# Kernel optimization log

Hardware: AMD Instinct MI355X
Metric: run time of the kernel (lower is better)

Reference implementation:

```python
import jax, jax.numpy as jnp
import numpy as np

NEG_SLOPE = 0.2

def setup_inputs() -> dict:
    key = jax.random.key(0)
    k1, k2, k3 = jax.random.split(key, 3)
    N, d, attn = 1024, 256, 256
    H = jax.random.normal(k1, (N, d), dtype=jnp.float32)
    # nn.Linear(2*d, attn, bias=False).weight has shape [attn, 2*d]
    W = jax.random.normal(k2, (attn, 2 * d), dtype=jnp.float32) * 0.05
    a = jax.random.normal(k3, (attn, 1), dtype=jnp.float32) * 0.05
    return {"H": H, "W": W, "a": a}

def reference(H, W, a):
    # Faithful to: E = leakyrelu(Linear(cat[H_i, H_j])); scores = E @ a; alpha = softmax(scores, dim=1); out = alpha @ H
    # Decompose W into halves acting on H_i and H_j to avoid the N x N x 2d concat:
    d = H.shape[1]
    W1, W2 = W[:, :d], W[:, d:]          # each [attn, d]
    Wh1 = H @ W1.T                        # [N, attn] (contribution of H_i)
    Wh2 = H @ W2.T                        # [N, attn] (contribution of H_j)
    E = jax.nn.leaky_relu(Wh1[:, None, :] + Wh2[None, :, :], NEG_SLOPE)  # [N, N, attn]
    scores = jnp.einsum('ijk,ko->ij', E, a)   # [N, N]
    alpha = jax.nn.softmax(scores, axis=1)    # softmax over j (dim=1)
    return alpha @ H                          # [N, d] weighted sum of H_j
```

## Files before the change

kernel.cpp:

```cpp
#include <hip/hip_runtime.h>


#define HALF 524288

__global__ __launch_bounds__(256) void k1_gemm_wh(const float* __restrict__ H,
                                                  const float* __restrict__ W,
                                                  float* __restrict__ Whp) {
    __shared__ float As[64][36];
    __shared__ float Bs[32][36];
    const int bi = blockIdx.x, bm = blockIdx.y, bz = blockIdx.z;
    const int t = threadIdx.x;
    const int ti = t >> 4, tj = t & 15;
    const int i0 = ti * 4;
    const int half = bm >> 3;
    const int kbase = bz * 128;
    float acc[4][2] = {};
    for (int kc = 0; kc < 128; kc += 32) {
        const int kg = kbase + kc;
        {
            const int r = t >> 2, c = (t & 3) * 8;
            *(float4*)&As[r][c] = *(const float4*)&H[(bi * 64 + r) * 256 + kg + c];
            *(float4*)&As[r][c + 4] =
                *(const float4*)&H[(bi * 64 + r) * 256 + kg + c + 4];
        }
        {
            const int r = t >> 3, c = (t & 7) * 4;
            const int wrow = (bm * 32 + r) & 255;
            *(float4*)&Bs[r][c] =
                *(const float4*)&W[wrow * 512 + half * 256 + kg + c];
        }
        __syncthreads();
#pragma unroll
        for (int k = 0; k < 32; k += 4) {
            float4 a[4], b[2];
#pragma unroll
            for (int r = 0; r < 4; ++r) a[r] = *(const float4*)&As[i0 + r][k];
#pragma unroll
            for (int c = 0; c < 2; ++c) b[c] = *(const float4*)&Bs[tj + 16 * c][k];
#pragma unroll
            for (int r = 0; r < 4; ++r)
#pragma unroll
                for (int c = 0; c < 2; ++c) {
                    acc[r][c] = fmaf(a[r].x, b[c].x, acc[r][c]);
                    acc[r][c] = fmaf(a[r].y, b[c].y, acc[r][c]);
                    acc[r][c] = fmaf(a[r].z, b[c].z, acc[r][c]);
                    acc[r][c] = fmaf(a[r].w, b[c].w, acc[r][c]);
                }
        }
        __syncthreads();
    }
    float* dst = Whp + (size_t)bz * HALF;
#pragma unroll
    for (int r = 0; r < 4; ++r)
#pragma unroll
        for (int c = 0; c < 2; ++c)
            dst[(size_t)(bi * 64 + i0 + r) * 512 + bm * 32 + tj + 16 * c] = acc[r][c];
}

__global__ __launch_bounds__(256) void k1b_s2(const float* __restrict__ Whp,
                                              const float* __restrict__ a,
                                              float* __restrict__ s2) {
    const int t = threadIdx.x;
    const int lane = t & 63, w = t >> 6;
    const int row = blockIdx.x * 4 + w;
    const size_t off = (size_t)row * 512 + 256 + lane * 4;
    float4 x0 = *(const float4*)&Whp[off];
    float4 x1 = *(const float4*)&Whp[HALF + off];
    float4 av = *(const float4*)&a[lane * 4];
    float d = (x0.x + x1.x) * av.x + (x0.y + x1.y) * av.y +
              (x0.z + x1.z) * av.z + (x0.w + x1.w) * av.w;
#pragma unroll
    for (int o = 32; o > 0; o >>= 1) d += __shfl_xor(d, o);
    if (lane == 0) s2[row] = 0.6f * d;
}

__global__ __launch_bounds__(256) void kF_flash(const float* __restrict__ Whp,
                                                const float* __restrict__ a,
                                                const float* __restrict__ s2,
                                                const float* __restrict__ H,
                                                float* __restrict__ avp,
                                                float* __restrict__ mbuf,
                                                float* __restrict__ lbuf) {
    __shared__ float X1[32][68];
    __shared__ float X2[64][68];
    __shared__ float P[32][68];
    __shared__ float bsh[256];
    const int bi = blockIdx.x, bj = blockIdx.y;
    const int t = threadIdx.x;
    const int ti = t >> 4, tj = t & 15;
    const int i0 = ti * 2;
    if (t < 64) {
        float4 av = *(const float4*)&a[t * 4];
        *(float4*)&bsh[t * 4] =
            make_float4(0.4f * av.x, 0.4f * av.y, 0.4f * av.z, 0.4f * av.w);
    }
    float acc[2][4] = {};
    for (int mc = 0; mc < 256; mc += 64) {
        {
            const int r = t >> 3, c = (t & 7) * 8;
            const size_t g = (size_t)(bi * 32 + r) * 512 + mc + c;
            float4 p0 = *(const float4*)&Whp[g];
            float4 p1 = *(const float4*)&Whp[HALF + g];
            *(float4*)&X1[r][c] =
                make_float4(p0.x + p1.x, p0.y + p1.y, p0.z + p1.z, p0.w + p1.w);
            float4 q0 = *(const float4*)&Whp[g + 4];
            float4 q1 = *(const float4*)&Whp[HALF + g + 4];
            *(float4*)&X1[r][c + 4] =
                make_float4(q0.x + q1.x, q0.y + q1.y, q0.z + q1.z, q0.w + q1.w);
        }
        {
            const int r = t >> 2, c = (t & 3) * 16;
            const size_t g = (size_t)(bj * 64 + r) * 512 + 256 + mc + c;
#pragma unroll
            for (int q = 0; q < 4; ++q) {
                float4 p0 = *(const float4*)&Whp[g + q * 4];
                float4 p1 = *(const float4*)&Whp[HALF + g + q * 4];
                *(float4*)&X2[r][c + q * 4] = make_float4(
                    p0.x + p1.x, p0.y + p1.y, p0.z + p1.z, p0.w + p1.w);
            }
        }
        __syncthreads();
#pragma unroll
        for (int k = 0; k < 64; k += 4) {
            float4 x1[2], x2[4];
#pragma unroll
            for (int r = 0; r < 2; ++r) x1[r] = *(const float4*)&X1[i0 + r][k];
#pragma unroll
            for (int c = 0; c < 4; ++c) x2[c] = *(const float4*)&X2[tj + 16 * c][k];
            const float4 bv = *(const float4*)&bsh[mc + k];
#pragma unroll
            for (int r = 0; r < 2; ++r)
#pragma unroll
                for (int c = 0; c < 4; ++c) {
                    acc[r][c] = fmaf(fabsf(x1[r].x + x2[c].x), bv.x, acc[r][c]);
                    acc[r][c] = fmaf(fabsf(x1[r].y + x2[c].y), bv.y, acc[r][c]);
                    acc[r][c] = fmaf(fabsf(x1[r].z + x2[c].z), bv.z, acc[r][c]);
                    acc[r][c] = fmaf(fabsf(x1[r].w + x2[c].w), bv.w, acc[r][c]);
                }
        }
        __syncthreads();
    }
#pragma unroll
    for (int c = 0; c < 4; ++c) {
        const float sv = s2[bj * 64 + tj + 16 * c];
        acc[0][c] += sv;
        acc[1][c] += sv;
    }
#pragma unroll
    for (int r = 0; r < 2; ++r) {
        float mm = fmaxf(fmaxf(acc[r][0], acc[r][1]), fmaxf(acc[r][2], acc[r][3]));
        mm = fmaxf(mm, __shfl_xor(mm, 1));
        mm = fmaxf(mm, __shfl_xor(mm, 2));
        mm = fmaxf(mm, __shfl_xor(mm, 4));
        mm = fmaxf(mm, __shfl_xor(mm, 8));
        float l0 = 0.f;
#pragma unroll
        for (int c = 0; c < 4; ++c) {
            acc[r][c] = __expf(acc[r][c] - mm);
            l0 += acc[r][c];
        }
        l0 += __shfl_xor(l0, 1);
        l0 += __shfl_xor(l0, 2);
        l0 += __shfl_xor(l0, 4);
        l0 += __shfl_xor(l0, 8);
#pragma unroll
        for (int c = 0; c < 4; ++c) P[i0 + r][tj + 16 * c] = acc[r][c];
        if (tj == 0) {
            const int gi = bi * 32 + i0 + r;
            mbuf[bj * 1024 + gi] = mm;
            lbuf[bj * 1024 + gi] = l0;
        }
    }
    __syncthreads();
    for (int cc = 0; cc < 256; cc += 64) {
        {
            const int r = t >> 2, c = (t & 3) * 16;
            const size_t g = (size_t)(bj * 64 + r) * 256 + cc + c;
#pragma unroll
            for (int q = 0; q < 4; ++q)
                *(float4*)&X2[r][c + q * 4] = *(const float4*)&H[g + q * 4];
        }
        __syncthreads();
        float acc2[2][4] = {};
#pragma unroll
        for (int jj = 0; jj < 64; jj += 4) {
            float4 pv[2], h[4];
#pragma unroll
            for (int r = 0; r < 2; ++r) pv[r] = *(const float4*)&P[i0 + r][jj];
#pragma unroll
            for (int q = 0; q < 4; ++q) h[q] = *(const float4*)&X2[jj + q][tj * 4];
#pragma unroll
            for (int r = 0; r < 2; ++r) {
                acc2[r][0] = fmaf(pv[r].x, h[0].x, acc2[r][0]);
                acc2[r][1] = fmaf(pv[r].x, h[0].y, acc2[r][1]);
                acc2[r][2] = fmaf(pv[r].x, h[0].z, acc2[r][2]);
                acc2[r][3] = fmaf(pv[r].x, h[0].w, acc2[r][3]);
                acc2[r][0] = fmaf(pv[r].y, h[1].x, acc2[r][0]);
                acc2[r][1] = fmaf(pv[r].y, h[1].y, acc2[r][1]);
                acc2[r][2] = fmaf(pv[r].y, h[1].z, acc2[r][2]);
                acc2[r][3] = fmaf(pv[r].y, h[1].w, acc2[r][3]);
                acc2[r][0] = fmaf(pv[r].z, h[2].x, acc2[r][0]);
                acc2[r][1] = fmaf(pv[r].z, h[2].y, acc2[r][1]);
                acc2[r][2] = fmaf(pv[r].z, h[2].z, acc2[r][2]);
                acc2[r][3] = fmaf(pv[r].z, h[2].w, acc2[r][3]);
                acc2[r][0] = fmaf(pv[r].w, h[3].x, acc2[r][0]);
                acc2[r][1] = fmaf(pv[r].w, h[3].y, acc2[r][1]);
                acc2[r][2] = fmaf(pv[r].w, h[3].z, acc2[r][2]);
                acc2[r][3] = fmaf(pv[r].w, h[3].w, acc2[r][3]);
            }
        }
#pragma unroll
        for (int r = 0; r < 2; ++r) {
            *(float4*)&avp[(size_t)bj * 262144 + (size_t)(bi * 32 + i0 + r) * 256 +
                           cc + tj * 4] =
                make_float4(acc2[r][0], acc2[r][1], acc2[r][2], acc2[r][3]);
        }
        __syncthreads();
    }
}

__global__ __launch_bounds__(256) void kM_merge(const float* __restrict__ avp,
                                                const float* __restrict__ mbuf,
                                                const float* __restrict__ lbuf,
                                                float* __restrict__ out) {
    const int t = threadIdx.x;
    const int i = blockIdx.x * 4 + (t >> 6);
    const int c0 = (t & 63) * 4;
    float ms[16], es[16];
    float M = -1e30f;
#pragma unroll
    for (int s = 0; s < 16; ++s) {
        ms[s] = mbuf[s * 1024 + i];
        M = fmaxf(M, ms[s]);
    }
    float L = 0.f;
#pragma unroll
    for (int s = 0; s < 16; ++s) {
        es[s] = __expf(ms[s] - M);
        L = fmaf(es[s], lbuf[s * 1024 + i], L);
    }
    const float inv = 1.0f / L;
    float4 o = make_float4(0.f, 0.f, 0.f, 0.f);
#pragma unroll
    for (int s = 0; s < 16; ++s) {
        float4 p = *(const float4*)&avp[(size_t)s * 262144 + (size_t)i * 256 + c0];
        o.x = fmaf(es[s], p.x, o.x);
        o.y = fmaf(es[s], p.y, o.y);
        o.z = fmaf(es[s], p.z, o.z);
        o.w = fmaf(es[s], p.w, o.w);
    }
    o.x *= inv; o.y *= inv; o.z *= inv; o.w *= inv;
    *(float4*)&out[(size_t)i * 256 + c0] = o;
}

extern "C" void kernel_launch(void* const* d_in, const int* in_sizes, int n_in,
                              void* d_out, int out_size, void* d_ws, size_t ws_size,
                              hipStream_t stream) {
    const float* H = (const float*)d_in[0];
    const float* W = (const float*)d_in[1];
    const float* a = (const float*)d_in[2];
    float* out = (float*)d_out;
    float* ws = (float*)d_ws;

    float* avp = ws;
    float* mbuf = ws + (4u << 20);
    float* lbuf = mbuf + 16384;
    float* Whp = lbuf + 16384;
    float* s2 = Whp + 2 * HALF;

    hipLaunchKernelGGL(k1_gemm_wh, dim3(16, 16, 2), dim3(256), 0, stream, H, W, Whp);
    hipLaunchKernelGGL(k1b_s2, dim3(256), dim3(256), 0, stream, Whp, a, s2);
    hipLaunchKernelGGL(kF_flash, dim3(32, 16), dim3(256), 0, stream, Whp, a, s2, H,
                       avp, mbuf, lbuf);
    hipLaunchKernelGGL(kM_merge, dim3(256), dim3(256), 0, stream, avp, mbuf, lbuf, out);
}
```

Before: 58.86 us.

## Pre-merge split-K partials and double-buffer flash kernel LDS tiles with register prefetch

The split-K partial sums of Wh are now added once in a dedicated merge kernel, which also computes s2, so the flash kernel reads a single Wh buffer instead of two partials per tile. The flash kernel double-buffers its X1/X2 and H tiles in shared memory and prefetches the next chunk into registers while computing the current one. Explicit waitcnt/barrier macros replace __syncthreads, and the s2 loads are hoisted. Whp now aliases the avp workspace, which is safe only because Whp is consumed before avp is written. The costs are more LDS per block, which may lower occupancy, and higher register pressure.

```diff
diff --git a/kernel.cpp b/kernel.cpp
--- a/kernel.cpp
+++ b/kernel.cpp
@@ -2,6 +2,21 @@
 
 
 #define HALF 524288
+#define LDW 68
+
+#define FENCE_BAR() do {                                   \
+    __builtin_amdgcn_sched_barrier(0);                     \
+    asm volatile("s_waitcnt lgkmcnt(0)" ::: "memory");     \
+    __builtin_amdgcn_s_barrier();                          \
+    __builtin_amdgcn_sched_barrier(0);                     \
+} while (0)
+
+#define BAR_ONLY() do {                                    \
+    __builtin_amdgcn_sched_barrier(0);                     \
+    asm volatile("s_waitcnt lgkmcnt(0)" ::: "memory");     \
+    __builtin_amdgcn_s_barrier();                          \
+    __builtin_amdgcn_sched_barrier(0);                     \
+} while (0)
 
 __global__ __launch_bounds__(256) void k1_gemm_wh(const float* __restrict__ H,
                                                   const float* __restrict__ W,
@@ -57,77 +72,104 @@
             dst[(size_t)(bi * 64 + i0 + r) * 512 + bm * 32 + tj + 16 * c] = acc[r][c];
 }
 
-__global__ __launch_bounds__(256) void k1b_s2(const float* __restrict__ Whp,
-                                              const float* __restrict__ a,
-                                              float* __restrict__ s2) {
+__global__ __launch_bounds__(256) void kW_merge(const float* __restrict__ Whp,
+                                                const float* __restrict__ a,
+                                                float* __restrict__ Wh,
+                                                float* __restrict__ s2) {
     const int t = threadIdx.x;
-    const int lane = t & 63, w = t >> 6;
-    const int row = blockIdx.x * 4 + w;
-    const size_t off = (size_t)row * 512 + 256 + lane * 4;
-    float4 x0 = *(const float4*)&Whp[off];
-    float4 x1 = *(const float4*)&Whp[HALF + off];
-    float4 av = *(const float4*)&a[lane * 4];
-    float d = (x0.x + x1.x) * av.x + (x0.y + x1.y) * av.y +
-              (x0.z + x1.z) * av.z + (x0.w + x1.w) * av.w;
-#pragma unroll
-    for (int o = 32; o > 0; o >>= 1) d += __shfl_xor(d, o);
-    if (lane == 0) s2[row] = 0.6f * d;
-}
-
-__global__ __launch_bounds__(256) void kF_flash(const float* __restrict__ Whp,
+    const int row = blockIdx.x * 2 + (t >> 7);
+    const int col = (t & 127) * 4;
+    const size_t off = (size_t)row * 512 + col;
+    float4 v0 = *(const float4*)&Whp[off];
+    float4 v1 = *(const float4*)&Whp[HALF + off];
+    float4 v = make_float4(v0.x + v1.x, v0.y + v1.y, v0.z + v1.z, v0.w + v1.w);
+    *(float4*)&Wh[off] = v;
+    if (col >= 256) {
+        float4 av = *(const float4*)&a[col - 256];
+        float p = av.x * v.x + av.y * v.y + av.z * v.z + av.w * v.w;
+#pragma unroll
+        for (int o = 32; o > 0; o >>= 1) p += __shfl_xor(p, o);
+        if ((t & 63) == 0) s2[row] = 0.6f * p;
+    }
+}
+
+__global__ __launch_bounds__(256) void kF_flash(const float* __restrict__ Wh,
                                                 const float* __restrict__ a,
                                                 const float* __restrict__ s2,
                                                 const float* __restrict__ H,
                                                 float* __restrict__ avp,
                                                 float* __restrict__ mbuf,
                                                 float* __restrict__ lbuf) {
-    __shared__ float X1[32][68];
-    __shared__ float X2[64][68];
-    __shared__ float P[32][68];
+    __shared__ float X1[2][32][LDW];
+    __shared__ float X2[2][64][LDW];
+    __shared__ float P[32][LDW];
     __shared__ float bsh[256];
     const int bi = blockIdx.x, bj = blockIdx.y;
     const int t = threadIdx.x;
     const int ti = t >> 4, tj = t & 15;
     const int i0 = ti * 2;
+    const int r1 = t >> 3, c1 = (t & 7) * 8;
+    const int r2 = t >> 2, c2 = (t & 3) * 16;
+    const float* g1 = Wh + (size_t)(bi * 32 + r1) * 512 + c1;
+    const float* g2 = Wh + (size_t)(bj * 64 + r2) * 512 + 256 + c2;
+    const float* gH = H + (size_t)(bj * 64 + r2) * 256 + c2;
+
+    float4 A0, A1, A2, A3, A4, A5, B0, B1, B2, B3, B4, B5;
+
+#define LOADC_A(mc) do { A0 = *(const float4*)(g1 + (mc)*64); \
+    A1 = *(const float4*)(g1 + (mc)*64 + 4);                  \
+    A2 = *(const float4*)(g2 + (mc)*64);                      \
+    A3 = *(const float4*)(g2 + (mc)*64 + 4);                  \
+    A4 = *(const float4*)(g2 + (mc)*64 + 8);                  \
+    A5 = *(const float4*)(g2 + (mc)*64 + 12); } while (0)
+#define LOADC_B(mc) do { B0 = *(const float4*)(g1 + (mc)*64); \
+    B1 = *(const float4*)(g1 + (mc)*64 + 4);                  \
+    B2 = *(const float4*)(g2 + (mc)*64);                      \
+    B3 = *(const float4*)(g2 + (mc)*64 + 4);                  \
+    B4 = *(const float4*)(g2 + (mc)*64 + 8);                  \
+    B5 = *(const float4*)(g2 + (mc)*64 + 12); } while (0)
+#define WRITEC_A(buf) do { *(float4*)&X1[buf][r1][c1] = A0;   \
+    *(float4*)&X1[buf][r1][c1 + 4] = A1;                      \
+    *(float4*)&X2[buf][r2][c2] = A2;                          \
+    *(float4*)&X2[buf][r2][c2 + 4] = A3;                      \
+    *(float4*)&X2[buf][r2][c2 + 8] = A4;                      \
+    *(float4*)&X2[buf][r2][c2 + 12] = A5; } while (0)
+#define WRITEC_B(buf) do { *(float4*)&X1[buf][r1][c1] = B0;   \
+    *(float4*)&X1[buf][r1][c1 + 4] = B1;                      \
+    *(float4*)&X2[buf][r2][c2] = B2;                          \
+    *(float4*)&X2[buf][r2][c2 + 4] = B3;                      \
+    *(float4*)&X2[buf][r2][c2 + 8] = B4;                      \
+    *(float4*)&X2[buf][r2][c2 + 12] = B5; } while (0)
+
+    LOADC_A(0);
+    float s2v0 = s2[bj * 64 + tj];
+    float s2v1 = s2[bj * 64 + tj + 16];
+    float s2v2 = s2[bj * 64 + tj + 32];
+    float s2v3 = s2[bj * 64 + tj + 48];
     if (t < 64) {
         float4 av = *(const float4*)&a[t * 4];
         *(float4*)&bsh[t * 4] =
             make_float4(0.4f * av.x, 0.4f * av.y, 0.4f * av.z, 0.4f * av.w);
     }
+
     float acc[2][4] = {};
-    for (int mc = 0; mc < 256; mc += 64) {
-        {
-            const int r = t >> 3, c = (t & 7) * 8;
-            const size_t g = (size_t)(bi * 32 + r) * 512 + mc + c;
-            float4 p0 = *(const float4*)&Whp[g];
-            float4 p1 = *(const float4*)&Whp[HALF + g];
-            *(float4*)&X1[r][c] =
-                make_float4(p0.x + p1.x, p0.y + p1.y, p0.z + p1.z, p0.w + p1.w);
-            float4 q0 = *(const float4*)&Whp[g + 4];
-            float4 q1 = *(const float4*)&Whp[HALF + g + 4];
-            *(float4*)&X1[r][c + 4] =
-                make_float4(q0.x + q1.x, q0.y + q1.y, q0.z + q1.z, q0.w + q1.w);
-        }
-        {
-            const int r = t >> 2, c = (t & 3) * 16;
-            const size_t g = (size_t)(bj * 64 + r) * 512 + 256 + mc + c;
-#pragma unroll
-            for (int q = 0; q < 4; ++q) {
-                float4 p0 = *(const float4*)&Whp[g + q * 4];
-                float4 p1 = *(const float4*)&Whp[HALF + g + q * 4];
-                *(float4*)&X2[r][c + q * 4] = make_float4(
-                    p0.x + p1.x, p0.y + p1.y, p0.z + p1.z, p0.w + p1.w);
-            }
-        }
-        __syncthreads();
+#pragma unroll
+    for (int mc = 0; mc < 4; ++mc) {
+        const int buf = mc & 1;
+        if (mc < 3) {
+            if (buf == 0) LOADC_B(mc + 1); else LOADC_A(mc + 1);
+        }
+        if (buf == 0) WRITEC_A(0); else WRITEC_B(1);
+        FENCE_BAR();
 #pragma unroll
         for (int k = 0; k < 64; k += 4) {
             float4 x1[2], x2[4];
 #pragma unroll
-            for (int r = 0; r < 2; ++r) x1[r] = *(const float4*)&X1[i0 + r][k];
-#pragma unroll
-            for (int c = 0; c < 4; ++c) x2[c] = *(const float4*)&X2[tj + 16 * c][k];
-            const float4 bv = *(const float4*)&bsh[mc + k];
+            for (int r = 0; r < 2; ++r) x1[r] = *(const float4*)&X1[buf][i0 + r][k];
+#pragma unroll
+            for (int c = 0; c < 4; ++c)
+                x2[c] = *(const float4*)&X2[buf][tj + 16 * c][k];
+            const float4 bv = *(const float4*)&bsh[mc * 64 + k];
 #pragma unroll
             for (int r = 0; r < 2; ++r)
 #pragma unroll
@@ -138,14 +180,20 @@
                     acc[r][c] = fmaf(fabsf(x1[r].w + x2[c].w), bv.w, acc[r][c]);
                 }
         }
-        __syncthreads();
-    }
-#pragma unroll
-    for (int c = 0; c < 4; ++c) {
-        const float sv = s2[bj * 64 + tj + 16 * c];
-        acc[0][c] += sv;
-        acc[1][c] += sv;
-    }
+        BAR_ONLY();
+    }
+
+    acc[0][0] += s2v0; acc[1][0] += s2v0;
+    acc[0][1] += s2v1; acc[1][1] += s2v1;
+    acc[0][2] += s2v2; acc[1][2] += s2v2;
+    acc[0][3] += s2v3; acc[1][3] += s2v3;
+
+    A2 = *(const float4*)(gH);
+    A3 = *(const float4*)(gH + 4);
+    A4 = *(const float4*)(gH + 8);
+    A5 = *(const float4*)(gH + 12);
+
+    float mm0, mm1, l00, l01;
 #pragma unroll
     for (int r = 0; r < 2; ++r) {
         float mm = fmaxf(fmaxf(acc[r][0], acc[r][1]), fmaxf(acc[r][2], acc[r][3]));
@@ -165,22 +213,38 @@
         l0 += __shfl_xor(l0, 8);
 #pragma unroll
         for (int c = 0; c < 4; ++c) P[i0 + r][tj + 16 * c] = acc[r][c];
-        if (tj == 0) {
-            const int gi = bi * 32 + i0 + r;
-            mbuf[bj * 1024 + gi] = mm;
-            lbuf[bj * 1024 + gi] = l0;
-        }
-    }
-    __syncthreads();
-    for (int cc = 0; cc < 256; cc += 64) {
-        {
-            const int r = t >> 2, c = (t & 3) * 16;
-            const size_t g = (size_t)(bj * 64 + r) * 256 + cc + c;
-#pragma unroll
-            for (int q = 0; q < 4; ++q)
-                *(float4*)&X2[r][c + q * 4] = *(const float4*)&H[g + q * 4];
-        }
-        __syncthreads();
+        if (r == 0) { mm0 = mm; l00 = l0; } else { mm1 = mm; l01 = l0; }
+    }
+    FENCE_BAR();
+
+#pragma unroll
+    for (int cc = 0; cc < 4; ++cc) {
+        const int buf = cc & 1;
+        if (cc < 3) {
+            if (buf == 0) {
+                B2 = *(const float4*)(gH + (cc + 1) * 64);
+                B3 = *(const float4*)(gH + (cc + 1) * 64 + 4);
+                B4 = *(const float4*)(gH + (cc + 1) * 64 + 8);
+                B5 = *(const float4*)(gH + (cc + 1) * 64 + 12);
+            } else {
+                A2 = *(const float4*)(gH + (cc + 1) * 64);
+                A3 = *(const float4*)(gH + (cc + 1) * 64 + 4);
+                A4 = *(const float4*)(gH + (cc + 1) * 64 + 8);
+                A5 = *(const float4*)(gH + (cc + 1) * 64 + 12);
+            }
+        }
+        if (buf == 0) {
+            *(float4*)&X2[0][r2][c2] = A2;
+            *(float4*)&X2[0][r2][c2 + 4] = A3;
+            *(float4*)&X2[0][r2][c2 + 8] = A4;
+            *(float4*)&X2[0][r2][c2 + 12] = A5;
+        } else {
+            *(float4*)&X2[1][r2][c2] = B2;
+            *(float4*)&X2[1][r2][c2 + 4] = B3;
+            *(float4*)&X2[1][r2][c2 + 8] = B4;
+            *(float4*)&X2[1][r2][c2 + 12] = B5;
+        }
+        FENCE_BAR();
         float acc2[2][4] = {};
 #pragma unroll
         for (int jj = 0; jj < 64; jj += 4) {
@@ -188,7 +252,8 @@
 #pragma unroll
             for (int r = 0; r < 2; ++r) pv[r] = *(const float4*)&P[i0 + r][jj];
 #pragma unroll
-            for (int q = 0; q < 4; ++q) h[q] = *(const float4*)&X2[jj + q][tj * 4];
+            for (int q = 0; q < 4; ++q)
+                h[q] = *(const float4*)&X2[buf][jj + q][tj * 4];
 #pragma unroll
             for (int r = 0; r < 2; ++r) {
                 acc2[r][0] = fmaf(pv[r].x, h[0].x, acc2[r][0]);
@@ -212,11 +277,22 @@
 #pragma unroll
         for (int r = 0; r < 2; ++r) {
             *(float4*)&avp[(size_t)bj * 262144 + (size_t)(bi * 32 + i0 + r) * 256 +
-                           cc + tj * 4] =
+                           cc * 64 + tj * 4] =
                 make_float4(acc2[r][0], acc2[r][1], acc2[r][2], acc2[r][3]);
         }
-        __syncthreads();
-    }
+        BAR_ONLY();
+    }
+    if (tj == 0) {
+        const int gi = bi * 32 + i0;
+        mbuf[bj * 1024 + gi] = mm0;
+        lbuf[bj * 1024 + gi] = l00;
+        mbuf[bj * 1024 + gi + 1] = mm1;
+        lbuf[bj * 1024 + gi + 1] = l01;
+    }
+#undef LOADC_A
+#undef LOADC_B
+#undef WRITEC_A
+#undef WRITEC_B
 }
 
 __global__ __launch_bounds__(256) void kM_merge(const float* __restrict__ avp,
@@ -263,14 +339,15 @@
     float* ws = (float*)d_ws;
 
     float* avp = ws;
-    float* mbuf = ws + (4u << 20);
+    float* Whp = ws;
+    float* Wh = ws + (4u << 20);
+    float* mbuf = Wh + HALF;
     float* lbuf = mbuf + 16384;
-    float* Whp = lbuf + 16384;
-    float* s2 = Whp + 2 * HALF;
+    float* s2 = lbuf + 16384;
 
     hipLaunchKernelGGL(k1_gemm_wh, dim3(16, 16, 2), dim3(256), 0, stream, H, W, Whp);
-    hipLaunchKernelGGL(k1b_s2, dim3(256), dim3(256), 0, stream, Whp, a, s2);
-    hipLaunchKernelGGL(kF_flash, dim3(32, 16), dim3(256), 0, stream, Whp, a, s2, H,
+    hipLaunchKernelGGL(kW_merge, dim3(512), dim3(256), 0, stream, Whp, a, Wh, s2);
+    hipLaunchKernelGGL(kF_flash, dim3(32, 16), dim3(256), 0, stream, Wh, a, s2, H,
                        avp, mbuf, lbuf);
     hipLaunchKernelGGL(kM_merge, dim3(256), dim3(256), 0, stream, avp, mbuf, lbuf, out);
 }
```

New measurement: 50.18 us. 14.8% less time.

## Double-buffer flash kernel with register prefetch and enlarge row tile to 64

Applied to the files above, without the earlier changes.

The main flash kernel now uses 64 rows per block instead of 32, with a 4x4 register tile per thread, which halves the grid and raises arithmetic reuse per shared-memory load. Global loads for the next chunk are prefetched into registers and written into double-buffered LDS, so a single barrier per step replaces the previous two. That barrier is a custom lgkmcnt wait. The first GEMM kernel now stages its whole 128-wide K slice into LDS at once and drops the inner K-chunk loop. The costs are more registers and LDS per block and fewer blocks in flight (256) on a large GPU.

```diff
diff --git a/kernel.cpp b/kernel.cpp
--- a/kernel.cpp
+++ b/kernel.cpp
@@ -2,59 +2,71 @@
 
 
 #define HALF 524288
+
+__device__ __forceinline__ float4 f4add(float4 a, float4 b) {
+    return make_float4(a.x + b.x, a.y + b.y, a.z + b.z, a.w + b.w);
+}
+
+#define LGKM_BAR() do {                                    \
+    __builtin_amdgcn_sched_barrier(0);                     \
+    asm volatile("s_waitcnt lgkmcnt(0)" ::: "memory");     \
+    __builtin_amdgcn_s_barrier();                          \
+    __builtin_amdgcn_sched_barrier(0);                     \
+} while (0)
 
 __global__ __launch_bounds__(256) void k1_gemm_wh(const float* __restrict__ H,
                                                   const float* __restrict__ W,
                                                   float* __restrict__ Whp) {
-    __shared__ float As[64][36];
-    __shared__ float Bs[32][36];
+    __shared__ float As[64 * 132];
+    __shared__ float Bs[32 * 132];
     const int bi = blockIdx.x, bm = blockIdx.y, bz = blockIdx.z;
     const int t = threadIdx.x;
     const int ti = t >> 4, tj = t & 15;
     const int i0 = ti * 4;
+    const int m0 = bm * 32;
     const int half = bm >> 3;
     const int kbase = bz * 128;
+    {
+        const int r = t >> 2, c = (t & 3) * 32;
+        const float* src = H + (size_t)(bi * 64 + r) * 256 + kbase + c;
+#pragma unroll
+        for (int q = 0; q < 8; ++q)
+            *(float4*)&As[r * 132 + c + q * 4] = *(const float4*)(src + q * 4);
+    }
+    {
+        const int r = t >> 3, c = (t & 7) * 16;
+        const float* src =
+            W + (size_t)((m0 + r) & 255) * 512 + half * 256 + kbase + c;
+#pragma unroll
+        for (int q = 0; q < 4; ++q)
+            *(float4*)&Bs[r * 132 + c + q * 4] = *(const float4*)(src + q * 4);
+    }
+    __syncthreads();
     float acc[4][2] = {};
-    for (int kc = 0; kc < 128; kc += 32) {
-        const int kg = kbase + kc;
-        {
-            const int r = t >> 2, c = (t & 3) * 8;
-            *(float4*)&As[r][c] = *(const float4*)&H[(bi * 64 + r) * 256 + kg + c];
-            *(float4*)&As[r][c + 4] =
-                *(const float4*)&H[(bi * 64 + r) * 256 + kg + c + 4];
-        }
-        {
-            const int r = t >> 3, c = (t & 7) * 4;
-            const int wrow = (bm * 32 + r) & 255;
-            *(float4*)&Bs[r][c] =
-                *(const float4*)&W[wrow * 512 + half * 256 + kg + c];
-        }
-        __syncthreads();
-#pragma unroll
-        for (int k = 0; k < 32; k += 4) {
-            float4 a[4], b[2];
-#pragma unroll
-            for (int r = 0; r < 4; ++r) a[r] = *(const float4*)&As[i0 + r][k];
-#pragma unroll
-            for (int c = 0; c < 2; ++c) b[c] = *(const float4*)&Bs[tj + 16 * c][k];
-#pragma unroll
-            for (int r = 0; r < 4; ++r)
-#pragma unroll
-                for (int c = 0; c < 2; ++c) {
-                    acc[r][c] = fmaf(a[r].x, b[c].x, acc[r][c]);
-                    acc[r][c] = fmaf(a[r].y, b[c].y, acc[r][c]);
-                    acc[r][c] = fmaf(a[r].z, b[c].z, acc[r][c]);
-                    acc[r][c] = fmaf(a[r].w, b[c].w, acc[r][c]);
-                }
-        }
-        __syncthreads();
+#pragma unroll 8
+    for (int k = 0; k < 128; k += 4) {
+        float4 a[4], b[2];
+#pragma unroll
+        for (int r = 0; r < 4; ++r) a[r] = *(const float4*)&As[(i0 + r) * 132 + k];
+#pragma unroll
+        for (int c = 0; c < 2; ++c)
+            b[c] = *(const float4*)&Bs[(tj + 16 * c) * 132 + k];
+#pragma unroll
+        for (int r = 0; r < 4; ++r)
+#pragma unroll
+            for (int c = 0; c < 2; ++c) {
+                acc[r][c] = fmaf(a[r].x, b[c].x, acc[r][c]);
+                acc[r][c] = fmaf(a[r].y, b[c].y, acc[r][c]);
+                acc[r][c] = fmaf(a[r].z, b[c].z, acc[r][c]);
+                acc[r][c] = fmaf(a[r].w, b[c].w, acc[r][c]);
+            }
     }
     float* dst = Whp + (size_t)bz * HALF;
 #pragma unroll
     for (int r = 0; r < 4; ++r)
 #pragma unroll
         for (int c = 0; c < 2; ++c)
-            dst[(size_t)(bi * 64 + i0 + r) * 512 + bm * 32 + tj + 16 * c] = acc[r][c];
+            dst[(size_t)(bi * 64 + i0 + r) * 512 + m0 + tj + 16 * c] = acc[r][c];
 }
 
 __global__ __launch_bounds__(256) void k1b_s2(const float* __restrict__ Whp,
@@ -81,55 +93,107 @@
                                                 float* __restrict__ avp,
                                                 float* __restrict__ mbuf,
                                                 float* __restrict__ lbuf) {
-    __shared__ float X1[32][68];
-    __shared__ float X2[64][68];
-    __shared__ float P[32][68];
+    __shared__ float R1[4608];
+    __shared__ float R2[4608];
     __shared__ float bsh[256];
     const int bi = blockIdx.x, bj = blockIdx.y;
     const int t = threadIdx.x;
     const int ti = t >> 4, tj = t & 15;
-    const int i0 = ti * 2;
+    const int i0 = ti * 4;
+    const int rs = t >> 2, cs = (t & 3) * 8;
+    const float* g1 = Whp + (size_t)(bi * 64 + rs) * 512 + cs;
+    const float* g2 = Whp + (size_t)(bj * 64 + rs) * 512 + 256 + cs;
+    const int cH = (t & 3) * 16;
+    const float* gH = H + (size_t)(bj * 64 + rs) * 256 + cH;
+
+    float4 A0, A1, A2, A3, A4, A5, A6, A7;
+    float4 B0, B1, B2, B3, B4, B5, B6, B7;
+
+#define LOADS_A(mc) do {                                     \
+    A0 = *(const float4*)(g1 + (mc) * 32);                   \
+    A1 = *(const float4*)(g1 + (mc) * 32 + 4);               \
+    A2 = *(const float4*)(g1 + HALF + (mc) * 32);            \
+    A3 = *(const float4*)(g1 + HALF + (mc) * 32 + 4);        \
+    A4 = *(const float4*)(g2 + (mc) * 32);                   \
+    A5 = *(const float4*)(g2 + (mc) * 32 + 4);               \
+    A6 = *(const float4*)(g2 + HALF + (mc) * 32);            \
+    A7 = *(const float4*)(g2 + HALF + (mc) * 32 + 4); } while (0)
+#define LOADS_B(mc) do {                                     \
+    B0 = *(const float4*)(g1 + (mc) * 32);                   \
+    B1 = *(const float4*)(g1 + (mc) * 32 + 4);               \
+    B2 = *(const float4*)(g1 + HALF + (mc) * 32);            \
+    B3 = *(const float4*)(g1 + HALF + (mc) * 32 + 4);        \
+    B4 = *(const float4*)(g2 + (mc) * 32);                   \
+    B5 = *(const float4*)(g2 + (mc) * 32 + 4);               \
+    B6 = *(const float4*)(g2 + HALF + (mc) * 32);            \
+    B7 = *(const float4*)(g2 + HALF + (mc) * 32 + 4); } while (0)
+#define WRITES_A(buf) do {                                   \
+    *(float4*)&R1[((buf) * 64 + rs) * 36 + cs] = f4add(A0, A2);      \
+    *(float4*)&R1[((buf) * 64 + rs) * 36 + cs + 4] = f4add(A1, A3);  \
+    *(float4*)&R2[((buf) * 64 + rs) * 36 + cs] = f4add(A4, A6);      \
+    *(float4*)&R2[((buf) * 64 + rs) * 36 + cs + 4] = f4add(A5, A7); } while (0)
+#define WRITES_B(buf) do {                                   \
+    *(float4*)&R1[((buf) * 64 + rs) * 36 + cs] = f4add(B0, B2);      \
+    *(float4*)&R1[((buf) * 64 + rs) * 36 + cs + 4] = f4add(B1, B3);  \
+    *(float4*)&R2[((buf) * 64 + rs) * 36 + cs] = f4add(B4, B6);      \
+    *(float4*)&R2[((buf) * 64 + rs) * 36 + cs + 4] = f4add(B5, B7); } while (0)
+#define LOADH_A(cc) do {                                     \
+    A0 = *(const float4*)(gH + (cc) * 64);                   \
+    A1 = *(const float4*)(gH + (cc) * 64 + 4);               \
+    A2 = *(const float4*)(gH + (cc) * 64 + 8);               \
+    A3 = *(const float4*)(gH + (cc) * 64 + 12); } while (0)
+#define LOADH_B(cc) do {                                     \
+    B0 = *(const float4*)(gH + (cc) * 64);                   \
+    B1 = *(const float4*)(gH + (cc) * 64 + 4);               \
+    B2 = *(const float4*)(gH + (cc) * 64 + 8);               \
+    B3 = *(const float4*)(gH + (cc) * 64 + 12); } while (0)
+#define WRITEH_A() do {                                      \
+    *(float4*)&R2[rs * 68 + cH] = A0;                        \
+    *(float4*)&R2[rs * 68 + cH + 4] = A1;                    \
+    *(float4*)&R2[rs * 68 + cH + 8] = A2;                    \
+    *(float4*)&R2[rs * 68 + cH + 12] = A3; } while (0)
+#define WRITEH_B() do {                                      \
+    *(float4*)&R2[rs * 68 + cH] = B0;                        \
+    *(float4*)&R2[rs * 68 + cH + 4] = B1;                    \
+    *(float4*)&R2[rs * 68 + cH + 8] = B2;                    \
+    *(float4*)&R2[rs * 68 + cH + 12] = B3; } while (0)
+
+    LOADS_A(0);
+    LOADS_B(1);
+    float s2v0 = s2[bj * 64 + tj];
+    float s2v1 = s2[bj * 64 + tj + 16];
+    float s2v2 = s2[bj * 64 + tj + 32];
+    float s2v3 = s2[bj * 64 + tj + 48];
     if (t < 64) {
         float4 av = *(const float4*)&a[t * 4];
         *(float4*)&bsh[t * 4] =
             make_float4(0.4f * av.x, 0.4f * av.y, 0.4f * av.z, 0.4f * av.w);
     }
-    float acc[2][4] = {};
-    for (int mc = 0; mc < 256; mc += 64) {
-        {
-            const int r = t >> 3, c = (t & 7) * 8;
-            const size_t g = (size_t)(bi * 32 + r) * 512 + mc + c;
-            float4 p0 = *(const float4*)&Whp[g];
-            float4 p1 = *(const float4*)&Whp[HALF + g];
-            *(float4*)&X1[r][c] =
-                make_float4(p0.x + p1.x, p0.y + p1.y, p0.z + p1.z, p0.w + p1.w);
-            float4 q0 = *(const float4*)&Whp[g + 4];
-            float4 q1 = *(const float4*)&Whp[HALF + g + 4];
-            *(float4*)&X1[r][c + 4] =
-                make_float4(q0.x + q1.x, q0.y + q1.y, q0.z + q1.z, q0.w + q1.w);
-        }
-        {
-            const int r = t >> 2, c = (t & 3) * 16;
-            const size_t g = (size_t)(bj * 64 + r) * 512 + 256 + mc + c;
-#pragma unroll
-            for (int q = 0; q < 4; ++q) {
-                float4 p0 = *(const float4*)&Whp[g + q * 4];
-                float4 p1 = *(const float4*)&Whp[HALF + g + q * 4];
-                *(float4*)&X2[r][c + q * 4] = make_float4(
-                    p0.x + p1.x, p0.y + p1.y, p0.z + p1.z, p0.w + p1.w);
-            }
-        }
-        __syncthreads();
-#pragma unroll
-        for (int k = 0; k < 64; k += 4) {
-            float4 x1[2], x2[4];
-#pragma unroll
-            for (int r = 0; r < 2; ++r) x1[r] = *(const float4*)&X1[i0 + r][k];
-#pragma unroll
-            for (int c = 0; c < 4; ++c) x2[c] = *(const float4*)&X2[tj + 16 * c][k];
-            const float4 bv = *(const float4*)&bsh[mc + k];
-#pragma unroll
-            for (int r = 0; r < 2; ++r)
+    WRITES_A(0);
+    LGKM_BAR();
+
+    float acc[4][4] = {};
+#pragma unroll
+    for (int mc = 0; mc < 8; ++mc) {
+        const int buf = mc & 1;
+        if (mc < 7) {
+            if (buf == 0) WRITES_B(1); else WRITES_A(0);
+        }
+        if (mc < 6) {
+            if (buf == 0) { LOADS_A(mc + 2); } else { LOADS_B(mc + 2); }
+        }
+#pragma unroll
+        for (int k = 0; k < 32; k += 4) {
+            float4 x1[4], x2[4];
+#pragma unroll
+            for (int r = 0; r < 4; ++r)
+                x1[r] = *(const float4*)&R1[(buf * 64 + i0 + r) * 36 + k];
+#pragma unroll
+            for (int c = 0; c < 4; ++c)
+                x2[c] = *(const float4*)&R2[(buf * 64 + tj + 16 * c) * 36 + k];
+            const float4 bv = *(const float4*)&bsh[mc * 32 + k];
+#pragma unroll
+            for (int r = 0; r < 4; ++r)
 #pragma unroll
                 for (int c = 0; c < 4; ++c) {
                     acc[r][c] = fmaf(fabsf(x1[r].x + x2[c].x), bv.x, acc[r][c]);
@@ -138,16 +202,18 @@
                     acc[r][c] = fmaf(fabsf(x1[r].w + x2[c].w), bv.w, acc[r][c]);
                 }
         }
-        __syncthreads();
-    }
-#pragma unroll
-    for (int c = 0; c < 4; ++c) {
-        const float sv = s2[bj * 64 + tj + 16 * c];
-        acc[0][c] += sv;
-        acc[1][c] += sv;
-    }
-#pragma unroll
-    for (int r = 0; r < 2; ++r) {
+        LGKM_BAR();
+    }
+
+#pragma unroll
+    for (int r = 0; r < 4; ++r) {
+        acc[r][0] += s2v0; acc[r][1] += s2v1;
+        acc[r][2] += s2v2; acc[r][3] += s2v3;
+    }
+    LOADH_A(0);
+    float mmv0, mmv1, mmv2, mmv3, llv0, llv1, llv2, llv3;
+#pragma unroll
+    for (int r = 0; r < 4; ++r) {
         float mm = fmaxf(fmaxf(acc[r][0], acc[r][1]), fmaxf(acc[r][2], acc[r][3]));
         mm = fmaxf(mm, __shfl_xor(mm, 1));
         mm = fmaxf(mm, __shfl_xor(mm, 2));
@@ -164,33 +230,33 @@
         l0 += __shfl_xor(l0, 4);
         l0 += __shfl_xor(l0, 8);
 #pragma unroll
-        for (int c = 0; c < 4; ++c) P[i0 + r][tj + 16 * c] = acc[r][c];
-        if (tj == 0) {
-            const int gi = bi * 32 + i0 + r;
-            mbuf[bj * 1024 + gi] = mm;
-            lbuf[bj * 1024 + gi] = l0;
-        }
-    }
-    __syncthreads();
-    for (int cc = 0; cc < 256; cc += 64) {
-        {
-            const int r = t >> 2, c = (t & 3) * 16;
-            const size_t g = (size_t)(bj * 64 + r) * 256 + cc + c;
+        for (int c = 0; c < 4; ++c) R1[(i0 + r) * 68 + tj + 16 * c] = acc[r][c];
+        if (r == 0) { mmv0 = mm; llv0 = l0; }
+        else if (r == 1) { mmv1 = mm; llv1 = l0; }
+        else if (r == 2) { mmv2 = mm; llv2 = l0; }
+        else { mmv3 = mm; llv3 = l0; }
+    }
+    LGKM_BAR();
+
+#pragma unroll
+    for (int cc = 0; cc < 4; ++cc) {
+        if ((cc & 1) == 0) WRITEH_A(); else WRITEH_B();
+        if (cc < 3) {
+            if ((cc & 1) == 0) { LOADH_B(cc + 1); } else { LOADH_A(cc + 1); }
+        }
+        LGKM_BAR();
+        float acc2[4][4] = {};
+#pragma unroll
+        for (int jj = 0; jj < 64; jj += 4) {
+            float4 pv[4], h[4];
+#pragma unroll
+            for (int r = 0; r < 4; ++r)
+                pv[r] = *(const float4*)&R1[(i0 + r) * 68 + jj];
 #pragma unroll
             for (int q = 0; q < 4; ++q)
-                *(float4*)&X2[r][c + q * 4] = *(const float4*)&H[g + q * 4];
-        }
-        __syncthreads();
-        float acc2[2][4] = {};
-#pragma unroll
-        for (int jj = 0; jj < 64; jj += 4) {
-            float4 pv[2], h[4];
-#pragma unroll
-            for (int r = 0; r < 2; ++r) pv[r] = *(const float4*)&P[i0 + r][jj];
-#pragma unroll
-            for (int q = 0; q < 4; ++q) h[q] = *(const float4*)&X2[jj + q][tj * 4];
-#pragma unroll
-            for (int r = 0; r < 2; ++r) {
+                h[q] = *(const float4*)&R2[(jj + q) * 68 + tj * 4];
+#pragma unroll
+            for (int r = 0; r < 4; ++r) {
                 acc2[r][0] = fmaf(pv[r].x, h[0].x, acc2[r][0]);
                 acc2[r][1] = fmaf(pv[r].x, h[0].y, acc2[r][1]);
                 acc2[r][2] = fmaf(pv[r].x, h[0].z, acc2[r][2]);
@@ -210,13 +276,28 @@
             }
         }
 #pragma unroll
-        for (int r = 0; r < 2; ++r) {
-            *(float4*)&avp[(size_t)bj * 262144 + (size_t)(bi * 32 + i0 + r) * 256 +
-                           cc + tj * 4] =
+        for (int r = 0; r < 4; ++r) {
+            *(float4*)&avp[(size_t)bj * 262144 +
+                           (size_t)(bi * 64 + i0 + r) * 256 + cc * 64 + tj * 4] =
                 make_float4(acc2[r][0], acc2[r][1], acc2[r][2], acc2[r][3]);
         }
-        __syncthreads();
-    }
+        LGKM_BAR();
+    }
+    if (tj == 0) {
+        const int gi = bi * 64 + i0;
+        mbuf[bj * 1024 + gi] = mmv0;     lbuf[bj * 1024 + gi] = llv0;
+        mbuf[bj * 1024 + gi + 1] = mmv1; lbuf[bj * 1024 + gi + 1] = llv1;
+        mbuf[bj * 1024 + gi + 2] = mmv2; lbuf[bj * 1024 + gi + 2] = llv2;
+        mbuf[bj * 1024 + gi + 3] = mmv3; lbuf[bj * 1024 + gi + 3] = llv3;
+    }
+#undef LOADS_A
+#undef LOADS_B
+#undef WRITES_A
+#undef WRITES_B
+#undef LOADH_A
+#undef LOADH_B
+#undef WRITEH_A
+#undef WRITEH_B
 }
 
 __global__ __launch_bounds__(256) void kM_merge(const float* __restrict__ avp,
@@ -263,14 +344,14 @@
     float* ws = (float*)d_ws;
 
     float* avp = ws;
-    float* mbuf = ws + (4u << 20);
+    float* Whp = ws + (4u << 20);
+    float* mbuf = Whp + 2 * HALF;
     float* lbuf = mbuf + 16384;
-    float* Whp = lbuf + 16384;
-    float* s2 = Whp + 2 * HALF;
+    float* s2 = lbuf + 16384;
 
     hipLaunchKernelGGL(k1_gemm_wh, dim3(16, 16, 2), dim3(256), 0, stream, H, W, Whp);
     hipLaunchKernelGGL(k1b_s2, dim3(256), dim3(256), 0, stream, Whp, a, s2);
-    hipLaunchKernelGGL(kF_flash, dim3(32, 16), dim3(256), 0, stream, Whp, a, s2, H,
+    hipLaunchKernelGGL(kF_flash, dim3(16, 16), dim3(256), 0, stream, Whp, a, s2, H,
                        avp, mbuf, lbuf);
     hipLaunchKernelGGL(kM_merge, dim3(256), dim3(256), 0, stream, avp, mbuf, lbuf, out);
 }
```

Measured after the change: 58.88 us. Within noise of the previous version (+0.0%).

## Drop split-K and LDS staging; read operands directly from global/L1 in GEMM and flash kernels

Applied to the files above, without the earlier changes.

The projection GEMM stops splitting K into two partial buffers, so each thread computes the full 256-long dot product and the downstream kernels no longer sum two partials. The LDS tiling and barriers in both the GEMM and the fused score/PV kernel are removed, and threads read their operand rows straight from global memory through the cache hierarchy. This cuts the partial-buffer traffic, the extra additions and the synchronisation. In exchange the reads are no longer shared through LDS, the per-thread access patterns are strided across rows, and the GEMM grid has half as many blocks.

```diff
diff --git a/kernel.cpp b/kernel.cpp
--- a/kernel.cpp
+++ b/kernel.cpp
@@ -1,88 +1,72 @@
 #include <hip/hip_runtime.h>
 
 
-#define HALF 524288
+__device__ __forceinline__ void f4fma(float4& acc, float s, float4 h) {
+    acc.x = fmaf(s, h.x, acc.x);
+    acc.y = fmaf(s, h.y, acc.y);
+    acc.z = fmaf(s, h.z, acc.z);
+    acc.w = fmaf(s, h.w, acc.w);
+}
 
 __global__ __launch_bounds__(256) void k1_gemm_wh(const float* __restrict__ H,
                                                   const float* __restrict__ W,
-                                                  float* __restrict__ Whp) {
-    __shared__ float As[64][36];
-    __shared__ float Bs[32][36];
-    const int bi = blockIdx.x, bm = blockIdx.y, bz = blockIdx.z;
+                                                  float* __restrict__ Wh) {
     const int t = threadIdx.x;
     const int ti = t >> 4, tj = t & 15;
-    const int i0 = ti * 4;
-    const int half = bm >> 3;
-    const int kbase = bz * 128;
+    const int ig = blockIdx.x * 64 + ti * 4;
+    const int mb = blockIdx.y * 32 + tj;
+    const int hf = blockIdx.y >> 3;
+    const int wr0 = mb & 255;
+    const int wr1 = (mb + 16) & 255;
+    const float* pa = H + (size_t)ig * 256;
+    const float* pb0 = W + (size_t)wr0 * 512 + hf * 256;
+    const float* pb1 = W + (size_t)wr1 * 512 + hf * 256;
     float acc[4][2] = {};
-    for (int kc = 0; kc < 128; kc += 32) {
-        const int kg = kbase + kc;
-        {
-            const int r = t >> 2, c = (t & 3) * 8;
-            *(float4*)&As[r][c] = *(const float4*)&H[(bi * 64 + r) * 256 + kg + c];
-            *(float4*)&As[r][c + 4] =
-                *(const float4*)&H[(bi * 64 + r) * 256 + kg + c + 4];
-        }
-        {
-            const int r = t >> 3, c = (t & 7) * 4;
-            const int wrow = (bm * 32 + r) & 255;
-            *(float4*)&Bs[r][c] =
-                *(const float4*)&W[wrow * 512 + half * 256 + kg + c];
-        }
-        __syncthreads();
-#pragma unroll
-        for (int k = 0; k < 32; k += 4) {
-            float4 a[4], b[2];
-#pragma unroll
-            for (int r = 0; r < 4; ++r) a[r] = *(const float4*)&As[i0 + r][k];
-#pragma unroll
-            for (int c = 0; c < 2; ++c) b[c] = *(const float4*)&Bs[tj + 16 * c][k];
-#pragma unroll
-            for (int r = 0; r < 4; ++r)
-#pragma unroll
-                for (int c = 0; c < 2; ++c) {
-                    acc[r][c] = fmaf(a[r].x, b[c].x, acc[r][c]);
-                    acc[r][c] = fmaf(a[r].y, b[c].y, acc[r][c]);
-                    acc[r][c] = fmaf(a[r].z, b[c].z, acc[r][c]);
-                    acc[r][c] = fmaf(a[r].w, b[c].w, acc[r][c]);
-                }
-        }
-        __syncthreads();
-    }
-    float* dst = Whp + (size_t)bz * HALF;
-#pragma unroll
-    for (int r = 0; r < 4; ++r)
-#pragma unroll
-        for (int c = 0; c < 2; ++c)
-            dst[(size_t)(bi * 64 + i0 + r) * 512 + bm * 32 + tj + 16 * c] = acc[r][c];
-}
-
-__global__ __launch_bounds__(256) void k1b_s2(const float* __restrict__ Whp,
+#pragma unroll 8
+    for (int k = 0; k < 256; k += 4) {
+        float4 b0 = *(const float4*)(pb0 + k);
+        float4 b1 = *(const float4*)(pb1 + k);
+        float4 a0 = *(const float4*)(pa + k);
+        float4 a1 = *(const float4*)(pa + 256 + k);
+        float4 a2 = *(const float4*)(pa + 512 + k);
+        float4 a3 = *(const float4*)(pa + 768 + k);
+        acc[0][0] += a0.x * b0.x + a0.y * b0.y + a0.z * b0.z + a0.w * b0.w;
+        acc[0][1] += a0.x * b1.x + a0.y * b1.y + a0.z * b1.z + a0.w * b1.w;
+        acc[1][0] += a1.x * b0.x + a1.y * b0.y + a1.z * b0.z + a1.w * b0.w;
+        acc[1][1] += a1.x * b1.x + a1.y * b1.y + a1.z * b1.z + a1.w * b1.w;
+        acc[2][0] += a2.x * b0.x + a2.y * b0.y + a2.z * b0.z + a2.w * b0.w;
+        acc[2][1] += a2.x * b1.x + a2.y * b1.y + a2.z * b1.z + a2.w * b1.w;
+        acc[3][0] += a3.x * b0.x + a3.y * b0.y + a3.z * b0.z + a3.w * b0.w;
+        acc[3][1] += a3.x * b1.x + a3.y * b1.y + a3.z * b1.z + a3.w * b1.w;
+    }
+#pragma unroll
+    for (int r = 0; r < 4; ++r) {
+        Wh[(size_t)(ig + r) * 512 + mb] = acc[r][0];
+        Wh[(size_t)(ig + r) * 512 + mb + 16] = acc[r][1];
+    }
+}
+
+__global__ __launch_bounds__(256) void k1b_s2(const float* __restrict__ Wh,
                                               const float* __restrict__ a,
                                               float* __restrict__ s2) {
     const int t = threadIdx.x;
     const int lane = t & 63, w = t >> 6;
     const int row = blockIdx.x * 4 + w;
-    const size_t off = (size_t)row * 512 + 256 + lane * 4;
-    float4 x0 = *(const float4*)&Whp[off];
-    float4 x1 = *(const float4*)&Whp[HALF + off];
+    float4 x = *(const float4*)&Wh[(size_t)row * 512 + 256 + lane * 4];
     float4 av = *(const float4*)&a[lane * 4];
-    float d = (x0.x + x1.x) * av.x + (x0.y + x1.y) * av.y +
-              (x0.z + x1.z) * av.z + (x0.w + x1.w) * av.w;
+    float d = x.x * av.x + x.y * av.y + x.z * av.z + x.w * av.w;
 #pragma unroll
     for (int o = 32; o > 0; o >>= 1) d += __shfl_xor(d, o);
     if (lane == 0) s2[row] = 0.6f * d;
 }
 
-__global__ __launch_bounds__(256) void kF_flash(const float* __restrict__ Whp,
+__global__ __launch_bounds__(256) void kF_flash(const float* __restrict__ Wh,
                                                 const float* __restrict__ a,
                                                 const float* __restrict__ s2,
                                                 const float* __restrict__ H,
                                                 float* __restrict__ avp,
                                                 float* __restrict__ mbuf,
                                                 float* __restrict__ lbuf) {
-    __shared__ float X1[32][68];
-    __shared__ float X2[64][68];
     __shared__ float P[32][68];
     __shared__ float bsh[256];
     const int bi = blockIdx.x, bj = blockIdx.y;
@@ -94,58 +78,66 @@
         *(float4*)&bsh[t * 4] =
             make_float4(0.4f * av.x, 0.4f * av.y, 0.4f * av.z, 0.4f * av.w);
     }
+    float s2v0 = s2[bj * 64 + tj];
+    float s2v1 = s2[bj * 64 + tj + 16];
+    float s2v2 = s2[bj * 64 + tj + 32];
+    float s2v3 = s2[bj * 64 + tj + 48];
+    const float* p1 = Wh + (size_t)(bi * 32 + i0) * 512;
+    const float* q0 = Wh + (size_t)(bj * 64 + tj) * 512 + 256;
+    const float* q1 = Wh + (size_t)(bj * 64 + tj + 16) * 512 + 256;
+    const float* q2 = Wh + (size_t)(bj * 64 + tj + 32) * 512 + 256;
+    const float* q3 = Wh + (size_t)(bj * 64 + tj + 48) * 512 + 256;
+    __syncthreads();
+
     float acc[2][4] = {};
-    for (int mc = 0; mc < 256; mc += 64) {
-        {
-            const int r = t >> 3, c = (t & 7) * 8;
-            const size_t g = (size_t)(bi * 32 + r) * 512 + mc + c;
-            float4 p0 = *(const float4*)&Whp[g];
-            float4 p1 = *(const float4*)&Whp[HALF + g];
-            *(float4*)&X1[r][c] =
-                make_float4(p0.x + p1.x, p0.y + p1.y, p0.z + p1.z, p0.w + p1.w);
-            float4 q0 = *(const float4*)&Whp[g + 4];
-            float4 q1 = *(const float4*)&Whp[HALF + g + 4];
-            *(float4*)&X1[r][c + 4] =
-                make_float4(q0.x + q1.x, q0.y + q1.y, q0.z + q1.z, q0.w + q1.w);
-        }
-        {
-            const int r = t >> 2, c = (t & 3) * 16;
-            const size_t g = (size_t)(bj * 64 + r) * 512 + 256 + mc + c;
-#pragma unroll
-            for (int q = 0; q < 4; ++q) {
-                float4 p0 = *(const float4*)&Whp[g + q * 4];
-                float4 p1 = *(const float4*)&Whp[HALF + g + q * 4];
-                *(float4*)&X2[r][c + q * 4] = make_float4(
-                    p0.x + p1.x, p0.y + p1.y, p0.z + p1.z, p0.w + p1.w);
-            }
-        }
-        __syncthreads();
-#pragma unroll
-        for (int k = 0; k < 64; k += 4) {
-            float4 x1[2], x2[4];
-#pragma unroll
-            for (int r = 0; r < 2; ++r) x1[r] = *(const float4*)&X1[i0 + r][k];
-#pragma unroll
-            for (int c = 0; c < 4; ++c) x2[c] = *(const float4*)&X2[tj + 16 * c][k];
-            const float4 bv = *(const float4*)&bsh[mc + k];
-#pragma unroll
-            for (int r = 0; r < 2; ++r)
-#pragma unroll
-                for (int c = 0; c < 4; ++c) {
-                    acc[r][c] = fmaf(fabsf(x1[r].x + x2[c].x), bv.x, acc[r][c]);
-                    acc[r][c] = fmaf(fabsf(x1[r].y + x2[c].y), bv.y, acc[r][c]);
-                    acc[r][c] = fmaf(fabsf(x1[r].z + x2[c].z), bv.z, acc[r][c]);
-                    acc[r][c] = fmaf(fabsf(x1[r].w + x2[c].w), bv.w, acc[r][c]);
-                }
-        }
-        __syncthreads();
-    }
-#pragma unroll
-    for (int c = 0; c < 4; ++c) {
-        const float sv = s2[bj * 64 + tj + 16 * c];
-        acc[0][c] += sv;
-        acc[1][c] += sv;
-    }
+#pragma unroll 8
+    for (int k = 0; k < 256; k += 4) {
+        float4 x1a = *(const float4*)(p1 + k);
+        float4 x1b = *(const float4*)(p1 + 512 + k);
+        float4 y0 = *(const float4*)(q0 + k);
+        float4 y1 = *(const float4*)(q1 + k);
+        float4 y2 = *(const float4*)(q2 + k);
+        float4 y3 = *(const float4*)(q3 + k);
+        const float4 bv = *(const float4*)&bsh[k];
+        acc[0][0] = fmaf(fabsf(x1a.x + y0.x), bv.x, acc[0][0]);
+        acc[0][0] = fmaf(fabsf(x1a.y + y0.y), bv.y, acc[0][0]);
+        acc[0][0] = fmaf(fabsf(x1a.z + y0.z), bv.z, acc[0][0]);
+        acc[0][0] = fmaf(fabsf(x1a.w + y0.w), bv.w, acc[0][0]);
+        acc[0][1] = fmaf(fabsf(x1a.x + y1.x), bv.x, acc[0][1]);
+        acc[0][1] = fmaf(fabsf(x1a.y + y1.y), bv.y, acc[0][1]);
+        acc[0][1] = fmaf(fabsf(x1a.z + y1.z), bv.z, acc[0][1]);
+        acc[0][1] = fmaf(fabsf(x1a.w + y1.w), bv.w, acc[0][1]);
+        acc[0][2] = fmaf(fabsf(x1a.x + y2.x), bv.x, acc[0][2]);
+        acc[0][2] = fmaf(fabsf(x1a.y + y2.y), bv.y, acc[0][2]);
+        acc[0][2] = fmaf(fabsf(x1a.z + y2.z), bv.z, acc[0][2]);
+        acc[0][2] = fmaf(fabsf(x1a.w + y2.w), bv.w, acc[0][2]);
+        acc[0][3] = fmaf(fabsf(x1a.x + y3.x), bv.x, acc[0][3]);
+        acc[0][3] = fmaf(fabsf(x1a.y + y3.y), bv.y, acc[0][3]);
+        acc[0][3] = fmaf(fabsf(x1a.z + y3.z), bv.z, acc[0][3]);
+        acc[0][3] = fmaf(fabsf(x1a.w + y3.w), bv.w, acc[0][3]);
+        acc[1][0] = fmaf(fabsf(x1b.x + y0.x), bv.x, acc[1][0]);
+        acc[1][0] = fmaf(fabsf(x1b.y + y0.y), bv.y, acc[1][0]);
+        acc[1][0] = fmaf(fabsf(x1b.z + y0.z), bv.z, acc[1][0]);
+        acc[1][0] = fmaf(fabsf(x1b.w + y0.w), bv.w, acc[1][0]);
+        acc[1][1] = fmaf(fabsf(x1b.x + y1.x), bv.x, acc[1][1]);
+        acc[1][1] = fmaf(fabsf(x1b.y + y1.y), bv.y, acc[1][1]);
+        acc[1][1] = fmaf(fabsf(x1b.z + y1.z), bv.z, acc[1][1]);
+        acc[1][1] = fmaf(fabsf(x1b.w + y1.w), bv.w, acc[1][1]);
+        acc[1][2] = fmaf(fabsf(x1b.x + y2.x), bv.x, acc[1][2]);
+        acc[1][2] = fmaf(fabsf(x1b.y + y2.y), bv.y, acc[1][2]);
+        acc[1][2] = fmaf(fabsf(x1b.z + y2.z), bv.z, acc[1][2]);
+        acc[1][2] = fmaf(fabsf(x1b.w + y2.w), bv.w, acc[1][2]);
+        acc[1][3] = fmaf(fabsf(x1b.x + y3.x), bv.x, acc[1][3]);
+        acc[1][3] = fmaf(fabsf(x1b.y + y3.y), bv.y, acc[1][3]);
+        acc[1][3] = fmaf(fabsf(x1b.z + y3.z), bv.z, acc[1][3]);
+        acc[1][3] = fmaf(fabsf(x1b.w + y3.w), bv.w, acc[1][3]);
+    }
+    acc[0][0] += s2v0; acc[1][0] += s2v0;
+    acc[0][1] += s2v1; acc[1][1] += s2v1;
+    acc[0][2] += s2v2; acc[1][2] += s2v2;
+    acc[0][3] += s2v3; acc[1][3] += s2v3;
+
+    float mm0, mm1, l00, l01;
 #pragma unroll
     for (int r = 0; r < 2; ++r) {
         float mm = fmaxf(fmaxf(acc[r][0], acc[r][1]), fmaxf(acc[r][2], acc[r][3]));
@@ -165,58 +157,51 @@
         l0 += __shfl_xor(l0, 8);
 #pragma unroll
         for (int c = 0; c < 4; ++c) P[i0 + r][tj + 16 * c] = acc[r][c];
-        if (tj == 0) {
-            const int gi = bi * 32 + i0 + r;
-            mbuf[bj * 1024 + gi] = mm;
-            lbuf[bj * 1024 + gi] = l0;
+        if (r == 0) { mm0 = mm; l00 = l0; } else { mm1 = mm; l01 = l0; }
+    }
+    if (tj == 0) {
+        const int gi = bi * 32 + i0;
+        mbuf[bj * 1024 + gi] = mm0;
+        lbuf[bj * 1024 + gi] = l00;
+        mbuf[bj * 1024 + gi + 1] = mm1;
+        lbuf[bj * 1024 + gi + 1] = l01;
+    }
+    __syncthreads();
+
+    const float* pH = H + (size_t)(bj * 64) * 256 + tj * 4;
+    float4 acc2[2][4] = {};
+#pragma unroll 4
+    for (int jj = 0; jj < 64; jj += 4) {
+        float4 pv0 = *(const float4*)&P[i0][jj];
+        float4 pv1 = *(const float4*)&P[i0 + 1][jj];
+#pragma unroll
+        for (int q = 0; q < 4; ++q) {
+            const float* hr = pH + (size_t)(jj + q) * 256;
+            float4 h0 = *(const float4*)(hr);
+            float4 h1 = *(const float4*)(hr + 64);
+            float4 h2 = *(const float4*)(hr + 128);
+            float4 h3 = *(const float4*)(hr + 192);
+            const float s0 = (q == 0) ? pv0.x : (q == 1) ? pv0.y
+                           : (q == 2) ? pv0.z : pv0.w;
+            const float s1 = (q == 0) ? pv1.x : (q == 1) ? pv1.y
+                           : (q == 2) ? pv1.z : pv1.w;
+            f4fma(acc2[0][0], s0, h0);
+            f4fma(acc2[0][1], s0, h1);
+            f4fma(acc2[0][2], s0, h2);
+            f4fma(acc2[0][3], s0, h3);
+            f4fma(acc2[1][0], s1, h0);
+            f4fma(acc2[1][1], s1, h1);
+            f4fma(acc2[1][2], s1, h2);
+            f4fma(acc2[1][3], s1, h3);
         }
     }
-    __syncthreads();
-    for (int cc = 0; cc < 256; cc += 64) {
-        {
-            const int r = t >> 2, c = (t & 3) * 16;
-            const size_t g = (size_t)(bj * 64 + r) * 256 + cc + c;
-#pragma unroll
-            for (int q = 0; q < 4; ++q)
-                *(float4*)&X2[r][c + q * 4] = *(const float4*)&H[g + q * 4];
-        }
-        __syncthreads();
-        float acc2[2][4] = {};
-#pragma unroll
-        for (int jj = 0; jj < 64; jj += 4) {
-            float4 pv[2], h[4];
-#pragma unroll
-            for (int r = 0; r < 2; ++r) pv[r] = *(const float4*)&P[i0 + r][jj];
-#pragma unroll
-            for (int q = 0; q < 4; ++q) h[q] = *(const float4*)&X2[jj + q][tj * 4];
-#pragma unroll
-            for (int r = 0; r < 2; ++r) {
-                acc2[r][0] = fmaf(pv[r].x, h[0].x, acc2[r][0]);
-                acc2[r][1] = fmaf(pv[r].x, h[0].y, acc2[r][1]);
-                acc2[r][2] = fmaf(pv[r].x, h[0].z, acc2[r][2]);
-                acc2[r][3] = fmaf(pv[r].x, h[0].w, acc2[r][3]);
-                acc2[r][0] = fmaf(pv[r].y, h[1].x, acc2[r][0]);
-                acc2[r][1] = fmaf(pv[r].y, h[1].y, acc2[r][1]);
-                acc2[r][2] = fmaf(pv[r].y, h[1].z, acc2[r][2]);
-                acc2[r][3] = fmaf(pv[r].y, h[1].w, acc2[r][3]);
-                acc2[r][0] = fmaf(pv[r].z, h[2].x, acc2[r][0]);
-                acc2[r][1] = fmaf(pv[r].z, h[2].y, acc2[r][1]);
-                acc2[r][2] = fmaf(pv[r].z, h[2].z, acc2[r][2]);
-                acc2[r][3] = fmaf(pv[r].z, h[2].w, acc2[r][3]);
-                acc2[r][0] = fmaf(pv[r].w, h[3].x, acc2[r][0]);
-                acc2[r][1] = fmaf(pv[r].w, h[3].y, acc2[r][1]);
-                acc2[r][2] = fmaf(pv[r].w, h[3].z, acc2[r][2]);
-                acc2[r][3] = fmaf(pv[r].w, h[3].w, acc2[r][3]);
-            }
-        }
-#pragma unroll
-        for (int r = 0; r < 2; ++r) {
-            *(float4*)&avp[(size_t)bj * 262144 + (size_t)(bi * 32 + i0 + r) * 256 +
-                           cc + tj * 4] =
-                make_float4(acc2[r][0], acc2[r][1], acc2[r][2], acc2[r][3]);
-        }
-        __syncthreads();
-    }
+#pragma unroll
+    for (int r = 0; r < 2; ++r)
+#pragma unroll
+        for (int cc = 0; cc < 4; ++cc)
+            *(float4*)&avp[(size_t)bj * 262144 +
+                           (size_t)(bi * 32 + i0 + r) * 256 + cc * 64 + tj * 4] =
+                acc2[r][cc];
 }
 
 __global__ __launch_bounds__(256) void kM_merge(const float* __restrict__ avp,
@@ -263,14 +248,14 @@
     float* ws = (float*)d_ws;
 
     float* avp = ws;
-    float* mbuf = ws + (4u << 20);
+    float* Wh = ws + (4u << 20);
+    float* mbuf = Wh + 524288;
     float* lbuf = mbuf + 16384;
-    float* Whp = lbuf + 16384;
-    float* s2 = Whp + 2 * HALF;
-
-    hipLaunchKernelGGL(k1_gemm_wh, dim3(16, 16, 2), dim3(256), 0, stream, H, W, Whp);
-    hipLaunchKernelGGL(k1b_s2, dim3(256), dim3(256), 0, stream, Whp, a, s2);
-    hipLaunchKernelGGL(kF_flash, dim3(32, 16), dim3(256), 0, stream, Whp, a, s2, H,
+    float* s2 = lbuf + 16384;
+
+    hipLaunchKernelGGL(k1_gemm_wh, dim3(16, 16), dim3(256), 0, stream, H, W, Wh);
+    hipLaunchKernelGGL(k1b_s2, dim3(256), dim3(256), 0, stream, Wh, a, s2);
+    hipLaunchKernelGGL(kF_flash, dim3(32, 16), dim3(256), 0, stream, Wh, a, s2, H,
                        avp, mbuf, lbuf);
     hipLaunchKernelGGL(kM_merge, dim3(256), dim3(256), 0, stream, avp, mbuf, lbuf, out);
 }
```

Measured after the change: 131.5 us. 2.23x slower.
